# Kernel optimization log

Measured on AMD Instinct MI355X. Metric: run time of the kernel, lower is better.

The kernel has to match this reference:

```python
import jax, jax.numpy as jnp
import numpy as np

B, P, K, HE, HF = 256, 128, 512, 1024, 512
D = K + HE + 2 * HF  # 2560, MLP input dim
HID = 64


def setup_inputs() -> dict:
    key = jax.random.key(0)
    ks = jax.random.split(key, 6)
    query = jax.random.normal(ks[0], (B, 1, HE), dtype=jnp.float32)
    keys = jax.random.normal(ks[1], (B, P, K), dtype=jnp.float32)
    frameLSTM_h = jax.random.normal(ks[2], (B, 1, 2 * HF), dtype=jnp.float32)
    mask = jax.random.randint(ks[3], (B, P), 0, 2, dtype=jnp.int32)
    mask = mask.at[:, 0].set(1)  # guarantee at least one unmasked player per row
    W1 = jax.random.normal(ks[4], (D, HID), dtype=jnp.float32) / np.float32(np.sqrt(D))
    W2 = jax.random.normal(ks[5], (HID, 1), dtype=jnp.float32) / np.float32(np.sqrt(HID))
    return dict(query=query, keys=keys, frameLSTM_h=frameLSTM_h, mask=mask, W1=W1, W2=W2)


def reference(query, keys, frameLSTM_h, mask, W1, W2):
    # Faithful to: cat([keys, query.repeat, frame.repeat]) @ W1 -> ReLU -> @ W2.
    # The pre-activation is linear, so splitting W1 by row-blocks is exactly the
    # same math without materializing the repeated/concatenated (B,P,D) tensor.
    W1k = W1[:K]            # (K, 64)
    W1q = W1[K:K + HE]      # (HE, 64)
    W1f = W1[K + HE:]       # (2*HF, 64)
    h = jax.nn.relu(
        jnp.einsum('bpk,kh->bph', keys, W1k)
        + jnp.einsum('boe,eh->boh', query, W1q)        # broadcasts over P
        + jnp.einsum('bof,fh->boh', frameLSTM_h, W1f)  # broadcasts over P
    )  # (B, P, 64)
    raw_scores = jnp.einsum('bph,ho->bp', h, W2)  # (B, P)
    raw_scores = jnp.where(mask == 0, -jnp.inf, raw_scores)
    weights = jax.nn.softmax(raw_scores, axis=1)  # (B, P)
    context = jnp.einsum('bp,bpk->bk', weights, keys)[:, None, :]  # (B, 1, K)
    embeddings = jnp.concatenate([context, frameLSTM_h], axis=2)   # (B, 1, K+2*HF)
    return embeddings, weights
```

## Files before the change

kernel.cpp:

```cpp
#include <hip/hip_runtime.h>
#include <hip/hip_bf16.h>
#include <cstdint>
#include <math.h>


typedef __bf16 bf16;
typedef __attribute__((ext_vector_type(8))) __bf16 bf16x8;
typedef __attribute__((ext_vector_type(4))) float f32x4;

#define NB 256
#define NP 128
#define NK 512
#define SMEM_BYTES (65536 + 8192 + 8192 + 512 + 512)

__global__ __launch_bounds__(512, 2) void fused_kernel(
    const float* __restrict__ keys, const float* __restrict__ query,
    const float* __restrict__ frame, const int* __restrict__ mask,
    const float* __restrict__ W1, const float* __restrict__ W2,
    float* __restrict__ out)
{
    extern __shared__ char smem[];
    char* sB      = smem;
    float* sq     = (float*)(smem + 65536);
    float* aux    = sq + 2048;
    float* scores = aux + 2048;
    float* wts    = scores + 128;

    const int b = blockIdx.x;
    const int t = threadIdx.x;
    const int w = t >> 6;
    const int lane = t & 63;
    const int m = lane & 15;
    const int q = lane >> 4;
    const int p0 = w * 16;
    const int xorv = (m & 7) << 4;

    {
        const int d = t * 4;
        const float* src = (d < 1024) ? (query + (size_t)b * 1024 + d)
                                      : (frame + (size_t)b * 1024 + (d - 1024));
        *(float4*)&sq[d] = *(const float4*)src;
    }

    {
#pragma unroll
        for (int i = 0; i < 8; i++) {
            const int id = t + 512 * i;
            const int h = id & 63;
            const int kc = id >> 6;
            float v[8];
#pragma unroll
            for (int j = 0; j < 8; j++)
                v[j] = W1[(size_t)(kc * 8 + j) * 64 + h];
            bf16x8 bv;
#pragma unroll
            for (int j = 0; j < 8; j++) bv[j] = (bf16)v[j];
            *(bf16x8*)(sB + ((h * 1024 + kc * 16) ^ ((h & 7) << 4))) = bv;
        }
    }
    __syncthreads();

    {
        const int s = t >> 4;
        const int j = t & 15;
        const float4* w1f4 = (const float4*)W1;
        float4 pa = {0.f, 0.f, 0.f, 0.f};
#pragma unroll
        for (int bt = 0; bt < 8; bt++) {
            float4 vv[8];
#pragma unroll
            for (int i = 0; i < 8; i++)
                vv[i] = w1f4[(size_t)(512 + s * 64 + bt * 8 + i) * 16 + j];
#pragma unroll
            for (int i = 0; i < 8; i++) {
                const float qv = sq[s * 64 + bt * 8 + i];
                pa.x += qv * vv[i].x; pa.y += qv * vv[i].y;
                pa.z += qv * vv[i].z; pa.w += qv * vv[i].w;
            }
        }
        pa.x += __shfl_xor(pa.x, 16); pa.y += __shfl_xor(pa.y, 16);
        pa.z += __shfl_xor(pa.z, 16); pa.w += __shfl_xor(pa.w, 16);
        pa.x += __shfl_xor(pa.x, 32); pa.y += __shfl_xor(pa.y, 32);
        pa.z += __shfl_xor(pa.z, 32); pa.w += __shfl_xor(pa.w, 32);
        if (lane < 16)
            *(float4*)&aux[w * 64 + lane * 4] = pa;
    }
    __syncthreads();

    float pv[4], wv[4];
#pragma unroll
    for (int nt = 0; nt < 4; nt++) {
        const int h = nt * 16 + m;
        float sacc = 0.f;
#pragma unroll
        for (int ww = 0; ww < 8; ww++) sacc += aux[ww * 64 + h];
        pv[nt] = sacc;
        wv[nt] = W2[h];
    }

    const float* arow = keys + (size_t)b * (NP * NK) + (size_t)(p0 + m) * NK + q * 8;
    float4 Aa[8], Ab[8];
#pragma unroll
    for (int i = 0; i < 6; i++) {
        Aa[i] = *(const float4*)(arow + i * 32);
        Ab[i] = *(const float4*)(arow + i * 32 + 4);
    }

    f32x4 acc[4];
#pragma unroll
    for (int nt = 0; nt < 4; nt++) acc[nt] = (f32x4){0.f, 0.f, 0.f, 0.f};

    bf16x8 Bp[2][4];
#pragma unroll
    for (int nt = 0; nt < 4; nt++)
        Bp[0][nt] = *(const bf16x8*)(sB + nt * 16384 + m * 1024 + ((q * 16) ^ xorv));

#pragma unroll
    for (int kk = 0; kk < 16; kk++) {
        const int cur = kk & 7;
        const int bc = kk & 1;
        if (kk < 10) {
            Aa[(kk + 6) & 7] = *(const float4*)(arow + (kk + 6) * 32);
            Ab[(kk + 6) & 7] = *(const float4*)(arow + (kk + 6) * 32 + 4);
        }
        if (kk < 15) {
#pragma unroll
            for (int nt = 0; nt < 4; nt++)
                Bp[bc ^ 1][nt] = *(const bf16x8*)(sB + nt * 16384 + m * 1024
                                  + ((((kk + 1) * 64) | (q * 16)) ^ xorv));
        }
        bf16x8 Af;
        Af[0] = (bf16)Aa[cur].x; Af[1] = (bf16)Aa[cur].y;
        Af[2] = (bf16)Aa[cur].z; Af[3] = (bf16)Aa[cur].w;
        Af[4] = (bf16)Ab[cur].x; Af[5] = (bf16)Ab[cur].y;
        Af[6] = (bf16)Ab[cur].z; Af[7] = (bf16)Ab[cur].w;
#pragma unroll
        for (int nt = 0; nt < 4; nt++)
            acc[nt] = __builtin_amdgcn_mfma_f32_16x16x32_bf16(Af, Bp[bc][nt], acc[nt], 0, 0, 0);
    }

    float pr[4] = {0.f, 0.f, 0.f, 0.f};
#pragma unroll
    for (int nt = 0; nt < 4; nt++)
#pragma unroll
        for (int r = 0; r < 4; r++)
            pr[r] += fmaxf(acc[nt][r] + pv[nt], 0.f) * wv[nt];

#pragma unroll
    for (int off = 1; off < 16; off <<= 1)
#pragma unroll
        for (int r = 0; r < 4; r++)
            pr[r] += __shfl_xor(pr[r], off);

    if (m == 0) {
#pragma unroll
        for (int r = 0; r < 4; r++) scores[p0 + q * 4 + r] = pr[r];
    }
    __syncthreads();

    const int cq = t & 127;
    const int pg = t >> 7;
    const float4* kp4 = (const float4*)(keys + (size_t)b * (NP * NK));
    float4 kv0[8];
#pragma unroll
    for (int i = 0; i < 8; i++)
        kv0[i] = kp4[(size_t)(pg * 32 + i) * 128 + cq];

    if (t < 64) {
        const int pa = t, pb = t + 64;
        float s0 = (mask[b * 128 + pa] == 0) ? -INFINITY : scores[pa];
        float s1 = (mask[b * 128 + pb] == 0) ? -INFINITY : scores[pb];
        float mx = fmaxf(s0, s1);
#pragma unroll
        for (int off = 32; off; off >>= 1) mx = fmaxf(mx, __shfl_xor(mx, off));
        float e0 = __expf(s0 - mx), e1 = __expf(s1 - mx);
        float sum = e0 + e1;
#pragma unroll
        for (int off = 32; off; off >>= 1) sum += __shfl_xor(sum, off);
        const float inv = 1.0f / sum;
        e0 *= inv; e1 *= inv;
        wts[pa] = e0; wts[pb] = e1;
        float* wout = out + (size_t)NB * 1536;
        wout[b * 128 + pa] = e0;
        wout[b * 128 + pb] = e1;
    }
    __syncthreads();

    {
        float4 ca = {0.f, 0.f, 0.f, 0.f};
#pragma unroll
        for (int i = 0; i < 8; i++) {
            const float wvv = wts[pg * 32 + i];
            ca.x += wvv * kv0[i].x; ca.y += wvv * kv0[i].y;
            ca.z += wvv * kv0[i].z; ca.w += wvv * kv0[i].w;
        }
#pragma unroll
        for (int bt = 1; bt < 4; bt++) {
            float4 kv[8];
#pragma unroll
            for (int i = 0; i < 8; i++)
                kv[i] = kp4[(size_t)(pg * 32 + bt * 8 + i) * 128 + cq];
#pragma unroll
            for (int i = 0; i < 8; i++) {
                const float wvv = wts[pg * 32 + bt * 8 + i];
                ca.x += wvv * kv[i].x; ca.y += wvv * kv[i].y;
                ca.z += wvv * kv[i].z; ca.w += wvv * kv[i].w;
            }
        }
        *(float4*)&aux[pg * 512 + cq * 4] = ca;
    }
    __syncthreads();
    {
        const int c = t;
        if (c < 512)
            out[(size_t)b * 1536 + c] =
                aux[c] + aux[512 + c] + aux[1024 + c] + aux[1536 + c];
    }
    if (t < 256) {
        const float4 fv = *(const float4*)(frame + (size_t)b * 1024 + t * 4);
        *(float4*)(out + (size_t)b * 1536 + 512 + t * 4) = fv;
    }
}

extern "C" void kernel_launch(void* const* d_in, const int* in_sizes, int n_in,
                              void* d_out, int out_size, void* d_ws, size_t ws_size,
                              hipStream_t stream) {
    const float* query = (const float*)d_in[0];
    const float* keys  = (const float*)d_in[1];
    const float* frame = (const float*)d_in[2];
    const int*   mask  = (const int*)d_in[3];
    const float* W1    = (const float*)d_in[4];
    const float* W2    = (const float*)d_in[5];
    float* out = (float*)d_out;

    hipFuncSetAttribute((const void*)fused_kernel,
                        hipFuncAttributeMaxDynamicSharedMemorySize, SMEM_BYTES);

    fused_kernel<<<256, 512, SMEM_BYTES, stream>>>(keys, query, frame, mask,
                                                   W1, W2, out);
}
```

Measured before the change: 118.5 us.

## Specialize waves: MFMA score waves overlap with query/frame projection waves

Splits the eight waves of each block into two groups. Waves 0-3 each compute scores for 32 players (two 16-row MFMA tiles sharing the B fragments). Waves 4-7 concurrently compute the query/frame projection onto W1, each covering twice as much of the reduction as before. This removes the serial projection phase and its barrier ahead of the key GEMM, so the two run in parallel. In exchange each MFMA wave carries double the accumulator and prefetch registers, fewer waves issue key loads, and the code relies on __syncthreads calls placed inside divergent branches matching up at the hardware barrier.

```diff
diff --git a/kernel.cpp b/kernel.cpp
--- a/kernel.cpp
+++ b/kernel.cpp
@@ -32,7 +32,6 @@
     const int lane = t & 63;
     const int m = lane & 15;
     const int q = lane >> 4;
-    const int p0 = w * 16;
     const int xorv = (m & 7) << 4;
 
     {
@@ -58,22 +57,110 @@
             *(bf16x8*)(sB + ((h * 1024 + kc * 16) ^ ((h & 7) << 4))) = bv;
         }
     }
-    __syncthreads();
-
-    {
-        const int s = t >> 4;
-        const int j = t & 15;
+
+    const int p0 = (w & 3) * 32;
+    const float* arow0 = keys + (size_t)b * (NP * NK) + (size_t)(p0 + m) * NK + q * 8;
+    const float* arow1 = arow0 + 16 * NK;
+    float4 A0a[4], A0b[4], A1a[4], A1b[4];
+    if (w < 4) {
+#pragma unroll
+        for (int i = 0; i < 3; i++) {
+            A0a[i] = *(const float4*)(arow0 + i * 32);
+            A0b[i] = *(const float4*)(arow0 + i * 32 + 4);
+            A1a[i] = *(const float4*)(arow1 + i * 32);
+            A1b[i] = *(const float4*)(arow1 + i * 32 + 4);
+        }
+    }
+    __syncthreads();
+
+    if (w < 4) {
+        f32x4 acc0[4], acc1[4];
+#pragma unroll
+        for (int nt = 0; nt < 4; nt++) {
+            acc0[nt] = (f32x4){0.f, 0.f, 0.f, 0.f};
+            acc1[nt] = (f32x4){0.f, 0.f, 0.f, 0.f};
+        }
+        bf16x8 Bp[2][4];
+#pragma unroll
+        for (int nt = 0; nt < 4; nt++)
+            Bp[0][nt] = *(const bf16x8*)(sB + nt * 16384 + m * 1024 + ((q * 16) ^ xorv));
+
+#pragma unroll
+        for (int kk = 0; kk < 16; kk++) {
+            const int cur = kk & 3;
+            const int bc = kk & 1;
+            if (kk < 13) {
+                A0a[(kk + 3) & 3] = *(const float4*)(arow0 + (kk + 3) * 32);
+                A0b[(kk + 3) & 3] = *(const float4*)(arow0 + (kk + 3) * 32 + 4);
+                A1a[(kk + 3) & 3] = *(const float4*)(arow1 + (kk + 3) * 32);
+                A1b[(kk + 3) & 3] = *(const float4*)(arow1 + (kk + 3) * 32 + 4);
+            }
+            if (kk < 15) {
+#pragma unroll
+                for (int nt = 0; nt < 4; nt++)
+                    Bp[bc ^ 1][nt] = *(const bf16x8*)(sB + nt * 16384 + m * 1024
+                                      + ((((kk + 1) * 64) | (q * 16)) ^ xorv));
+            }
+            bf16x8 Af0, Af1;
+            Af0[0] = (bf16)A0a[cur].x; Af0[1] = (bf16)A0a[cur].y;
+            Af0[2] = (bf16)A0a[cur].z; Af0[3] = (bf16)A0a[cur].w;
+            Af0[4] = (bf16)A0b[cur].x; Af0[5] = (bf16)A0b[cur].y;
+            Af0[6] = (bf16)A0b[cur].z; Af0[7] = (bf16)A0b[cur].w;
+            Af1[0] = (bf16)A1a[cur].x; Af1[1] = (bf16)A1a[cur].y;
+            Af1[2] = (bf16)A1a[cur].z; Af1[3] = (bf16)A1a[cur].w;
+            Af1[4] = (bf16)A1b[cur].x; Af1[5] = (bf16)A1b[cur].y;
+            Af1[6] = (bf16)A1b[cur].z; Af1[7] = (bf16)A1b[cur].w;
+#pragma unroll
+            for (int nt = 0; nt < 4; nt++) {
+                acc0[nt] = __builtin_amdgcn_mfma_f32_16x16x32_bf16(Af0, Bp[bc][nt], acc0[nt], 0, 0, 0);
+                acc1[nt] = __builtin_amdgcn_mfma_f32_16x16x32_bf16(Af1, Bp[bc][nt], acc1[nt], 0, 0, 0);
+            }
+        }
+        __syncthreads();
+
+        float pr0[4] = {0.f, 0.f, 0.f, 0.f};
+        float pr1[4] = {0.f, 0.f, 0.f, 0.f};
+#pragma unroll
+        for (int nt = 0; nt < 4; nt++) {
+            const int h = nt * 16 + m;
+            const float pvh = aux[h] + aux[64 + h] + aux[128 + h] + aux[192 + h];
+            const float wvh = W2[h];
+#pragma unroll
+            for (int r = 0; r < 4; r++) {
+                pr0[r] += fmaxf(acc0[nt][r] + pvh, 0.f) * wvh;
+                pr1[r] += fmaxf(acc1[nt][r] + pvh, 0.f) * wvh;
+            }
+        }
+#pragma unroll
+        for (int off = 1; off < 16; off <<= 1)
+#pragma unroll
+            for (int r = 0; r < 4; r++) {
+                pr0[r] += __shfl_xor(pr0[r], off);
+                pr1[r] += __shfl_xor(pr1[r], off);
+            }
+        if (m == 0) {
+#pragma unroll
+            for (int r = 0; r < 4; r++) {
+                scores[p0 + q * 4 + r] = pr0[r];
+                scores[p0 + 16 + q * 4 + r] = pr1[r];
+            }
+        }
+    } else {
+        const int wp = w - 4;
+        const int s4 = lane >> 4;
+        const int j = lane & 15;
+        const int d0 = wp * 512 + s4 * 128;
         const float4* w1f4 = (const float4*)W1;
         float4 pa = {0.f, 0.f, 0.f, 0.f};
 #pragma unroll
-        for (int bt = 0; bt < 8; bt++) {
+        for (int bt = 0; bt < 16; bt++) {
             float4 vv[8];
 #pragma unroll
             for (int i = 0; i < 8; i++)
-                vv[i] = w1f4[(size_t)(512 + s * 64 + bt * 8 + i) * 16 + j];
+                vv[i] = w1f4[(size_t)(512 + d0 + bt * 8 + i) * 16 + j];
 #pragma unroll
             for (int i = 0; i < 8; i++) {
-                const float qv = sq[s * 64 + bt * 8 + i];
+                const float qv = sq[d0 + bt * 8 + i];
                 pa.x += qv * vv[i].x; pa.y += qv * vv[i].y;
                 pa.z += qv * vv[i].z; pa.w += qv * vv[i].w;
             }
@@ -83,78 +170,8 @@
         pa.x += __shfl_xor(pa.x, 32); pa.y += __shfl_xor(pa.y, 32);
         pa.z += __shfl_xor(pa.z, 32); pa.w += __shfl_xor(pa.w, 32);
         if (lane < 16)
-            *(float4*)&aux[w * 64 + lane * 4] = pa;
-    }
-    __syncthreads();
-
-    float pv[4], wv[4];
-#pragma unroll
-    for (int nt = 0; nt < 4; nt++) {
-        const int h = nt * 16 + m;
-        float sacc = 0.f;
-#pragma unroll
-        for (int ww = 0; ww < 8; ww++) sacc += aux[ww * 64 + h];
-        pv[nt] = sacc;
-        wv[nt] = W2[h];
-    }
-
-    const float* arow = keys + (size_t)b * (NP * NK) + (size_t)(p0 + m) * NK + q * 8;
-    float4 Aa[8], Ab[8];
-#pragma unroll
-    for (int i = 0; i < 6; i++) {
-        Aa[i] = *(const float4*)(arow + i * 32);
-        Ab[i] = *(const float4*)(arow + i * 32 + 4);
-    }
-
-    f32x4 acc[4];
-#pragma unroll
-    for (int nt = 0; nt < 4; nt++) acc[nt] = (f32x4){0.f, 0.f, 0.f, 0.f};
-
-    bf16x8 Bp[2][4];
-#pragma unroll
-    for (int nt = 0; nt < 4; nt++)
-        Bp[0][nt] = *(const bf16x8*)(sB + nt * 16384 + m * 1024 + ((q * 16) ^ xorv));
-
-#pragma unroll
-    for (int kk = 0; kk < 16; kk++) {
-        const int cur = kk & 7;
-        const int bc = kk & 1;
-        if (kk < 10) {
-            Aa[(kk + 6) & 7] = *(const float4*)(arow + (kk + 6) * 32);
-            Ab[(kk + 6) & 7] = *(const float4*)(arow + (kk + 6) * 32 + 4);
-        }
-        if (kk < 15) {
-#pragma unroll
-            for (int nt = 0; nt < 4; nt++)
-                Bp[bc ^ 1][nt] = *(const bf16x8*)(sB + nt * 16384 + m * 1024
-                                  + ((((kk + 1) * 64) | (q * 16)) ^ xorv));
-        }
-        bf16x8 Af;
-        Af[0] = (bf16)Aa[cur].x; Af[1] = (bf16)Aa[cur].y;
-        Af[2] = (bf16)Aa[cur].z; Af[3] = (bf16)Aa[cur].w;
-        Af[4] = (bf16)Ab[cur].x; Af[5] = (bf16)Ab[cur].y;
-        Af[6] = (bf16)Ab[cur].z; Af[7] = (bf16)Ab[cur].w;
-#pragma unroll
-        for (int nt = 0; nt < 4; nt++)
-            acc[nt] = __builtin_amdgcn_mfma_f32_16x16x32_bf16(Af, Bp[bc][nt], acc[nt], 0, 0, 0);
-    }
-
-    float pr[4] = {0.f, 0.f, 0.f, 0.f};
-#pragma unroll
-    for (int nt = 0; nt < 4; nt++)
-#pragma unroll
-        for (int r = 0; r < 4; r++)
-            pr[r] += fmaxf(acc[nt][r] + pv[nt], 0.f) * wv[nt];
-
-#pragma unroll
-    for (int off = 1; off < 16; off <<= 1)
-#pragma unroll
-        for (int r = 0; r < 4; r++)
-            pr[r] += __shfl_xor(pr[r], off);
-
-    if (m == 0) {
-#pragma unroll
-        for (int r = 0; r < 4; r++) scores[p0 + q * 4 + r] = pr[r];
+            *(float4*)&aux[wp * 64 + lane * 4] = pa;
+        __syncthreads();
     }
     __syncthreads();
 
@@ -167,9 +184,9 @@
         kv0[i] = kp4[(size_t)(pg * 32 + i) * 128 + cq];
 
     if (t < 64) {
-        const int pa = t, pb = t + 64;
-        float s0 = (mask[b * 128 + pa] == 0) ? -INFINITY : scores[pa];
-        float s1 = (mask[b * 128 + pb] == 0) ? -INFINITY : scores[pb];
+        const int pa_ = t, pb_ = t + 64;
+        float s0 = (mask[b * 128 + pa_] == 0) ? -INFINITY : scores[pa_];
+        float s1 = (mask[b * 128 + pb_] == 0) ? -INFINITY : scores[pb_];
         float mx = fmaxf(s0, s1);
 #pragma unroll
         for (int off = 32; off; off >>= 1) mx = fmaxf(mx, __shfl_xor(mx, off));
@@ -179,10 +196,10 @@
         for (int off = 32; off; off >>= 1) sum += __shfl_xor(sum, off);
         const float inv = 1.0f / sum;
         e0 *= inv; e1 *= inv;
-        wts[pa] = e0; wts[pb] = e1;
+        wts[pa_] = e0; wts[pb_] = e1;
         float* wout = out + (size_t)NB * 1536;
-        wout[b * 128 + pa] = e0;
-        wout[b * 128 + pb] = e1;
+        wout[b * 128 + pa_] = e0;
+        wout[b * 128 + pb_] = e1;
     }
     __syncthreads();
 
@@ -210,12 +227,10 @@
         *(float4*)&aux[pg * 512 + cq * 4] = ca;
     }
     __syncthreads();
-    {
-        const int c = t;
-        if (c < 512)
-            out[(size_t)b * 1536 + c] =
-                aux[c] + aux[512 + c] + aux[1024 + c] + aux[1536 + c];
-    }
+    if (t < 512)
+        out[(size_t)b * 1536 + t] =
+            aux[t] + aux[512 + t] + aux[1024 + t] + aux[1536 + t];
+
     if (t < 256) {
         const float4 fv = *(const float4*)(frame + (size_t)b * 1024 + t * 4);
         *(float4*)(out + (size_t)b * 1536 + 512 + t * 4) = fv;
```

New measurement: 123.7 us. 4.4% more time.

## Stage keys tiles through per-wave LDS double buffer for MFMA A operand

Applied to the files above, without the earlier changes.

The keys A-operand is now loaded in coalesced, XOR-swizzled 64-column chunks into a per-wave 8KB LDS double buffer, then read back from LDS to build the bf16 fragments. Previously each lane loaded its strided row segments straight into a deep register prefetch ring. The aim is wider contiguous global accesses and lower register pressure. In exchange it adds LDS writes and reads, reduces the prefetch depth to one chunk ahead, and grows shared memory by 64KB per block.

```diff
diff --git a/kernel.cpp b/kernel.cpp
--- a/kernel.cpp
+++ b/kernel.cpp
@@ -11,7 +11,7 @@
 #define NB 256
 #define NP 128
 #define NK 512
-#define SMEM_BYTES (65536 + 8192 + 8192 + 512 + 512)
+#define SMEM_BYTES (65536 + 8192 + 8192 + 512 + 512 + 65536)
 
 __global__ __launch_bounds__(512, 2) void fused_kernel(
     const float* __restrict__ keys, const float* __restrict__ query,
@@ -25,6 +25,7 @@
     float* aux    = sq + 2048;
     float* scores = aux + 2048;
     float* wts    = scores + 128;
+    char* kb      = smem + 65536 + 8192 + 8192 + 1024;
 
     const int b = blockIdx.x;
     const int t = threadIdx.x;
@@ -58,6 +59,15 @@
             *(bf16x8*)(sB + ((h * 1024 + kc * 16) ^ ((h & 7) << 4))) = bv;
         }
     }
+
+    const float* kbase = keys + (size_t)b * (NP * NK);
+    float4 kvs[4];
+#pragma unroll
+    for (int s = 0; s < 4; s++) {
+        const int rl = s * 4 + (lane >> 4);
+        const int cc = (lane & 15) ^ (rl & 7);
+        kvs[s] = *(const float4*)(kbase + (size_t)(p0 + rl) * NK + cc * 4);
+    }
     __syncthreads();
 
     {
@@ -98,13 +108,10 @@
         wv[nt] = W2[h];
     }
 
-    const float* arow = keys + (size_t)b * (NP * NK) + (size_t)(p0 + m) * NK + q * 8;
-    float4 Aa[8], Ab[8];
-#pragma unroll
-    for (int i = 0; i < 6; i++) {
-        Aa[i] = *(const float4*)(arow + i * 32);
-        Ab[i] = *(const float4*)(arow + i * 32 + 4);
-    }
+    char* kbw = kb + w * 8192;
+#pragma unroll
+    for (int s = 0; s < 4; s++)
+        *(float4*)(kbw + s * 1024 + lane * 16) = kvs[s];
 
     f32x4 acc[4];
 #pragma unroll
@@ -116,27 +123,45 @@
         Bp[0][nt] = *(const bf16x8*)(sB + nt * 16384 + m * 1024 + ((q * 16) ^ xorv));
 
 #pragma unroll
-    for (int kk = 0; kk < 16; kk++) {
-        const int cur = kk & 7;
-        const int bc = kk & 1;
-        if (kk < 10) {
-            Aa[(kk + 6) & 7] = *(const float4*)(arow + (kk + 6) * 32);
-            Ab[(kk + 6) & 7] = *(const float4*)(arow + (kk + 6) * 32 + 4);
-        }
-        if (kk < 15) {
+    for (int c = 0; c < 8; c++) {
+        if (c < 7) {
+#pragma unroll
+            for (int s = 0; s < 4; s++) {
+                const int rl = s * 4 + (lane >> 4);
+                const int cc = (lane & 15) ^ (rl & 7);
+                kvs[s] = *(const float4*)(kbase + (size_t)(p0 + rl) * NK
+                                          + (c + 1) * 64 + cc * 4);
+            }
+        }
+        const char* kbr = kbw + (c & 1) * 4096;
+#pragma unroll
+        for (int kk2 = 0; kk2 < 2; kk2++) {
+            const int kkg = c * 2 + kk2;
+            const int bc = kkg & 1;
+            const int a0 = (m * 256 + kk2 * 128 + q * 32) ^ xorv;
+            const float4 f0 = *(const float4*)(kbr + a0);
+            const float4 f1 = *(const float4*)(kbr + (a0 ^ 16));
+            if (kkg < 15) {
+#pragma unroll
+                for (int nt = 0; nt < 4; nt++)
+                    Bp[bc ^ 1][nt] = *(const bf16x8*)(sB + nt * 16384 + m * 1024
+                                      + ((((kkg + 1) * 64) | (q * 16)) ^ xorv));
+            }
+            bf16x8 Af;
+            Af[0] = (bf16)f0.x; Af[1] = (bf16)f0.y;
+            Af[2] = (bf16)f0.z; Af[3] = (bf16)f0.w;
+            Af[4] = (bf16)f1.x; Af[5] = (bf16)f1.y;
+            Af[6] = (bf16)f1.z; Af[7] = (bf16)f1.w;
 #pragma unroll
             for (int nt = 0; nt < 4; nt++)
-                Bp[bc ^ 1][nt] = *(const bf16x8*)(sB + nt * 16384 + m * 1024
-                                  + ((((kk + 1) * 64) | (q * 16)) ^ xorv));
-        }
-        bf16x8 Af;
-        Af[0] = (bf16)Aa[cur].x; Af[1] = (bf16)Aa[cur].y;
-        Af[2] = (bf16)Aa[cur].z; Af[3] = (bf16)Aa[cur].w;
-        Af[4] = (bf16)Ab[cur].x; Af[5] = (bf16)Ab[cur].y;
-        Af[6] = (bf16)Ab[cur].z; Af[7] = (bf16)Ab[cur].w;
-#pragma unroll
-        for (int nt = 0; nt < 4; nt++)
-            acc[nt] = __builtin_amdgcn_mfma_f32_16x16x32_bf16(Af, Bp[bc][nt], acc[nt], 0, 0, 0);
+                acc[nt] = __builtin_amdgcn_mfma_f32_16x16x32_bf16(Af, Bp[bc][nt], acc[nt], 0, 0, 0);
+        }
+        if (c < 7) {
+            char* kbwn = kbw + ((c + 1) & 1) * 4096;
+#pragma unroll
+            for (int s = 0; s < 4; s++)
+                *(float4*)(kbwn + s * 1024 + lane * 16) = kvs[s];
+        }
     }
 
     float pr[4] = {0.f, 0.f, 0.f, 0.f};
@@ -160,16 +185,16 @@
 
     const int cq = t & 127;
     const int pg = t >> 7;
-    const float4* kp4 = (const float4*)(keys + (size_t)b * (NP * NK));
+    const float4* kp4 = (const float4*)kbase;
     float4 kv0[8];
 #pragma unroll
     for (int i = 0; i < 8; i++)
         kv0[i] = kp4[(size_t)(pg * 32 + i) * 128 + cq];
 
     if (t < 64) {
-        const int pa = t, pb = t + 64;
-        float s0 = (mask[b * 128 + pa] == 0) ? -INFINITY : scores[pa];
-        float s1 = (mask[b * 128 + pb] == 0) ? -INFINITY : scores[pb];
+        const int pa_ = t, pb_ = t + 64;
+        float s0 = (mask[b * 128 + pa_] == 0) ? -INFINITY : scores[pa_];
+        float s1 = (mask[b * 128 + pb_] == 0) ? -INFINITY : scores[pb_];
         float mx = fmaxf(s0, s1);
 #pragma unroll
         for (int off = 32; off; off >>= 1) mx = fmaxf(mx, __shfl_xor(mx, off));
@@ -179,10 +204,10 @@
         for (int off = 32; off; off >>= 1) sum += __shfl_xor(sum, off);
         const float inv = 1.0f / sum;
         e0 *= inv; e1 *= inv;
-        wts[pa] = e0; wts[pb] = e1;
+        wts[pa_] = e0; wts[pb_] = e1;
         float* wout = out + (size_t)NB * 1536;
-        wout[b * 128 + pa] = e0;
-        wout[b * 128 + pb] = e1;
+        wout[b * 128 + pa_] = e0;
+        wout[b * 128 + pb_] = e1;
     }
     __syncthreads();
 
@@ -210,12 +235,10 @@
         *(float4*)&aux[pg * 512 + cq * 4] = ca;
     }
     __syncthreads();
-    {
-        const int c = t;
-        if (c < 512)
-            out[(size_t)b * 1536 + c] =
-                aux[c] + aux[512 + c] + aux[1024 + c] + aux[1536 + c];
-    }
+    if (t < 512)
+        out[(size_t)b * 1536 + t] =
+            aux[t] + aux[512 + t] + aux[1024 + t] + aux[1536 + t];
+
     if (t < 256) {
         const float4 fv = *(const float4*)(frame + (size_t)b * 1024 + t * 4);
         *(float4*)(out + (size_t)b * 1536 + 512 + t * 4) = fv;
```

After: 123.4 us. 4.2% more time.
